# Kernel tuning notes

Hardware: AMD Instinct MI355X
Metric: run time of the kernel (lower is better)

## Reference

```python
import jax, jax.numpy as jnp
import numpy as np

E = 1024   # embd_size
H = 16     # head_count
HS = E // H
B = 8
T = 1024   # seq len == input_size
EPS = 1e-5

def _ln(x, g, b):
    m = jnp.mean(x, axis=-1, keepdims=True)
    v = jnp.mean((x - m) ** 2, axis=-1, keepdims=True)
    return (x - m) * jax.lax.rsqrt(v + EPS) * g + b

def setup_inputs() -> dict:
    key = jax.random.key(0)
    ks = jax.random.split(key, 12)
    s_attn = 1.0 / np.sqrt(E)
    s_ff1 = 1.0 / np.sqrt(E)
    s_ff2 = 1.0 / np.sqrt(4 * E)
    return {
        "x": jax.random.normal(ks[0], (B, T, E), dtype=jnp.float32),
        "wq": jax.random.normal(ks[1], (H, E, HS), dtype=jnp.float32) * s_attn,
        "wk": jax.random.normal(ks[2], (H, E, HS), dtype=jnp.float32) * s_attn,
        "wv": jax.random.normal(ks[3], (H, E, HS), dtype=jnp.float32) * s_attn,
        "w_proj": jax.random.normal(ks[4], (E, E), dtype=jnp.float32) * s_attn,
        "b_proj": jnp.zeros((E,), dtype=jnp.float32),
        "w1": jax.random.normal(ks[5], (E, 4 * E), dtype=jnp.float32) * s_ff1,
        "b1": jnp.zeros((4 * E,), dtype=jnp.float32),
        "w2": jax.random.normal(ks[6], (4 * E, E), dtype=jnp.float32) * s_ff2,
        "b2": jnp.zeros((E,), dtype=jnp.float32),
        "g1": jnp.ones((E,), dtype=jnp.float32),
        "be1": jnp.zeros((E,), dtype=jnp.float32),
        "g2": jnp.ones((E,), dtype=jnp.float32),
        "be2": jnp.zeros((E,), dtype=jnp.float32),
    }

def reference(x, wq, wk, wv, w_proj, b_proj, w1, b1, w2, b2, g1, be1, g2, be2):
    Tn = x.shape[1]
    h = _ln(x, g1, be1)
    # per-head projections, batched over heads: [B,T,E] x [H,E,S] -> [B,H,T,S]
    q = jnp.einsum('bte,hes->bhts', h, wq)
    k = jnp.einsum('bte,hes->bhts', h, wk)
    v = jnp.einsum('bte,hes->bhts', h, wv)
    scores = jnp.einsum('bhts,bhus->bhtu', q, k)
    # NOTE: source multiplies by sqrt(T) (x.shape[2] of scores), not 1/sqrt(head_size)
    scores = scores * jnp.float32(Tn) ** 0.5
    causal = jnp.tril(jnp.ones((Tn, Tn), dtype=bool))
    scores = jnp.where(causal, scores, -jnp.inf)
    attn = jax.nn.softmax(scores, axis=-1)
    out = jnp.einsum('bhtu,bhus->bhts', attn, v)           # [B,H,T,S]
    out = out.transpose(0, 2, 1, 3).reshape(x.shape[0], Tn, E)  # concat heads
    out = out @ w_proj + b_proj
    x = x + out
    f = _ln(x, g2, be2)
    f = jax.nn.relu(f @ w1 + b1) @ w2 + b2
    return x + f
```

## Files before the change

kernel.cpp:

```cpp
#include <hip/hip_runtime.h>


typedef unsigned short u16;
typedef __attribute__((ext_vector_type(8))) short  bfx8;
typedef __attribute__((ext_vector_type(4))) float  f32x4;
typedef __attribute__((ext_vector_type(4))) unsigned short u16v4;

#define MFMA16 __builtin_amdgcn_mfma_f32_16x16x32_bf16

__device__ __forceinline__ u16 f2bf(float f) {
    union { float f; unsigned u; } c; c.f = f;
    unsigned r = c.u + 0x7fffu + ((c.u >> 16) & 1u);
    return (u16)(r >> 16);
}
__device__ __forceinline__ float bf2f(u16 b) {
    union { unsigned u; float f; } c; c.u = ((unsigned)b) << 16; return c.f;
}
__device__ __forceinline__ float exp2_fast(float x) {
    float r; asm("v_exp_f32 %0, %1" : "=v"(r) : "v"(x)); return r;
}

__device__ __forceinline__ void gl_lds16(const void* g, void* l) {
    void* gg = (void*)g;
    __builtin_amdgcn_global_load_lds(
        (__attribute__((address_space(1))) void*)gg,
        (__attribute__((address_space(3))) void*)l,
        16, 0, 0);
}

__global__ __launch_bounds__(256)
void transpose_split(const float* __restrict__ src, u16* __restrict__ dhi,
                     u16* __restrict__ dlo, int C, int OS,
                     size_t inBS, size_t outBS)
{
    __shared__ float t[64][65];
    const int tid = threadIdx.x;
    const float* s = src + (size_t)blockIdx.z * inBS
                   + ((size_t)blockIdx.y * 64) * C + (size_t)blockIdx.x * 64;
    const size_t obase = (size_t)blockIdx.z * outBS
                       + ((size_t)blockIdx.x * 64) * OS + (size_t)blockIdx.y * 64;
    {
        const int r = tid >> 2, c4 = (tid & 3) * 16;
#pragma unroll
        for (int k = 0; k < 4; ++k) {
            float4 f = *(const float4*)(s + (size_t)r * C + c4 + k * 4);
            t[r][c4 + k*4 + 0] = f.x; t[r][c4 + k*4 + 1] = f.y;
            t[r][c4 + k*4 + 2] = f.z; t[r][c4 + k*4 + 3] = f.w;
        }
    }
    __syncthreads();
    {
        const int c = tid >> 2, r4 = (tid & 3) * 16;
        bfx8 h0, h1, l0, l1;
#pragma unroll
        for (int k = 0; k < 8; ++k) {
            float v0 = t[r4 + k][c];
            float v1 = t[r4 + 8 + k][c];
            u16 a = f2bf(v0), b = f2bf(v1);
            h0[k] = (short)a; h1[k] = (short)b;
            l0[k] = (short)f2bf(v0 - bf2f(a));
            l1[k] = (short)f2bf(v1 - bf2f(b));
        }
        u16* d = dhi + obase + (size_t)c * OS + r4;
        *(bfx8*)d = h0; *(bfx8*)(d + 8) = h1;
        if (dlo) {
            u16* d2 = dlo + obase + (size_t)c * OS + r4;
            *(bfx8*)d2 = l0; *(bfx8*)(d2 + 8) = l1;
        }
    }
}

__global__ __launch_bounds__(256)
void transpose_v(const u16* __restrict__ v, u16* __restrict__ vT)
{
    const int ut = blockIdx.x, h = blockIdx.y, b = blockIdx.z;
    __shared__ u16 t[64][72];
    const int tid = threadIdx.x;
    {
        const int u = tid >> 2, s4 = (tid & 3) * 16;
        const u16* src = v + ((size_t)(b * 1024 + ut * 64 + u)) * 1024 + h * 64 + s4;
        bfx8 a = *(const bfx8*)src;
        bfx8 c = *(const bfx8*)(src + 8);
#pragma unroll
        for (int k = 0; k < 8; ++k) { t[u][s4 + k] = (u16)a[k]; t[u][s4 + 8 + k] = (u16)c[k]; }
    }
    __syncthreads();
    {
        const int s = tid >> 2, u4 = (tid & 3) * 16;
        bfx8 o0, o1;
#pragma unroll
        for (int k = 0; k < 8; ++k) { o0[k] = (short)t[u4 + k][s]; o1[k] = (short)t[u4 + 8 + k][s]; }
        u16* dst = vT + ((size_t)((b * 16 + h) * 64 + s)) * 1024 + ut * 64 + u4;
        *(bfx8*)dst = o0; *(bfx8*)(dst + 8) = o1;
    }
}

__global__ __launch_bounds__(256)
void ln_split(const float* __restrict__ x, const float* __restrict__ g,
              const float* __restrict__ be, u16* __restrict__ hhi,
              u16* __restrict__ hlo)
{
    const int row = blockIdx.x;
    const int tid = threadIdx.x;
    const float4 v = ((const float4*)(x + (size_t)row * 1024))[tid];
    float s  = v.x + v.y + v.z + v.w;
    float s2 = v.x*v.x + v.y*v.y + v.z*v.z + v.w*v.w;
#pragma unroll
    for (int m = 32; m >= 1; m >>= 1) {
        s  += __shfl_xor(s,  m, 64);
        s2 += __shfl_xor(s2, m, 64);
    }
    __shared__ float rs[4], rq[4];
    if ((tid & 63) == 0) { rs[tid >> 6] = s; rq[tid >> 6] = s2; }
    __syncthreads();
    s  = rs[0] + rs[1] + rs[2] + rs[3];
    s2 = rq[0] + rq[1] + rq[2] + rq[3];
    const float mean = s * (1.0f / 1024.0f);
    const float var  = s2 * (1.0f / 1024.0f) - mean * mean;
    const float inv  = rsqrtf(var + 1e-5f);
    const int col0 = tid * 4;
    float hv[4];
    hv[0] = (v.x - mean) * inv * g[col0+0] + be[col0+0];
    hv[1] = (v.y - mean) * inv * g[col0+1] + be[col0+1];
    hv[2] = (v.z - mean) * inv * g[col0+2] + be[col0+2];
    hv[3] = (v.w - mean) * inv * g[col0+3] + be[col0+3];
    u16v4 hb, lb;
#pragma unroll
    for (int k = 0; k < 4; ++k) {
        u16 a = f2bf(hv[k]);
        hb[k] = a;
        lb[k] = f2bf(hv[k] - bf2f(a));
    }
    *(u16v4*)(hhi + (size_t)row * 1024 + col0) = hb;
    if (hlo) *(u16v4*)(hlo + (size_t)row * 1024 + col0) = lb;
}

#define BM 128
#define BN 128
#define BKT 32

template<int FLAGS>
__global__ __launch_bounds__(256, 2)
void gemm_bt(const u16* __restrict__ A, const u16* __restrict__ Bt,
             void* __restrict__ Cout, const float* __restrict__ bias,
             const float* __restrict__ res, int M, int N, int K)
{
    __shared__ u16 As[BM * BKT];
    __shared__ u16 Bs[BN * BKT];
    const int tid  = threadIdx.x;
    const int lane = tid & 63, wave = tid >> 6;
    const int wr = wave >> 1, wc = wave & 1;
    const int li = lane & 15, lg = lane >> 4;
    const size_t m0 = (size_t)blockIdx.y * BM;
    const size_t n0 = (size_t)blockIdx.x * BN;
    f32x4 acc[4][4] = {};

    const int slot0 = tid, slot1 = tid + 256;
    const int r0 = slot0 >> 2, kc0 = (slot0 & 3) * 8;
    const int r1 = slot1 >> 2, kc1 = (slot1 & 3) * 8;

    for (int kt = 0; kt < K; kt += BKT) {
        __syncthreads();
        gl_lds16(A  + (m0 + r0) * K + kt + kc0, As + slot0 * 8);
        gl_lds16(Bt + (n0 + r0) * K + kt + kc0, Bs + slot0 * 8);
        gl_lds16(A  + (m0 + r1) * K + kt + kc1, As + slot1 * 8);
        gl_lds16(Bt + (n0 + r1) * K + kt + kc1, Bs + slot1 * 8);
        __syncthreads();
        bfx8 af[4], bfr[4];
#pragma unroll
        for (int i = 0; i < 4; ++i)
            af[i] = *(const bfx8*)&As[(wr * 64 + i * 16 + li) * BKT + lg * 8];
#pragma unroll
        for (int j = 0; j < 4; ++j)
            bfr[j] = *(const bfx8*)&Bs[(wc * 64 + j * 16 + li) * BKT + lg * 8];
#pragma unroll
        for (int i = 0; i < 4; ++i)
#pragma unroll
            for (int j = 0; j < 4; ++j)
                acc[i][j] = MFMA16(af[i], bfr[j], acc[i][j], 0, 0, 0);
    }

    float* Cf = (float*)Cout;
    u16*   Cb = (u16*)Cout;
#pragma unroll
    for (int i = 0; i < 4; ++i)
#pragma unroll
        for (int j = 0; j < 4; ++j)
#pragma unroll
            for (int r = 0; r < 4; ++r) {
                const size_t row = m0 + wr * 64 + i * 16 + lg * 4 + r;
                const size_t col = n0 + wc * 64 + j * 16 + li;
                float v = acc[i][j][r];
                if (FLAGS & 1) v += bias[col];
                if (FLAGS & 2) v = fmaxf(v, 0.0f);
                if (FLAGS & 4) v += res[row * (size_t)N + col];
                if (FLAGS & 8) Cf[row * (size_t)N + col] = v;
                else           Cb[row * (size_t)N + col] = f2bf(v);
            }
}

__global__ __launch_bounds__(512, 2)
void gemm8_ffn1(const u16* __restrict__ A, const u16* __restrict__ Bt,
                u16* __restrict__ C, const float* __restrict__ bias,
                int M, int N, int K)
{
    __shared__ u16 Asl[2][2][128 * 64];
    __shared__ u16 Bsl[2][2][128 * 64];
    const int tid = threadIdx.x;
    const int lane = tid & 63, wave = tid >> 6;
    const int wr = wave >> 2, wc = wave & 3;
    const int li = lane & 15, lg = lane >> 4;

    const int bid = blockIdx.x;
    const int swz = (bid & 7) * 64 + (bid >> 3);
    const int bx = swz & 15, by = swz >> 4;
    const size_t m0 = (size_t)by * 256, n0 = (size_t)bx * 256;

    char* ldsA = (char*)&Asl[0][0][0];
    char* ldsB = (char*)&Bsl[0][0][0];

    auto stageA = [&](int j, int h) {
#pragma unroll
        for (int site = 0; site < 2; ++site) {
            const int s = tid + site * 512;
            const int r = s >> 3;
            const int cb = ((s & 7) << 4) ^ ((r & 7) << 4);
            gl_lds16((const char*)(A + (m0 + h * 128 + r) * (size_t)K + (size_t)j * 64) + cb,
                     ldsA + ((j & 1) * 2 + h) * 16384 + s * 16);
        }
    };
    auto stageB = [&](int j, int h) {
#pragma unroll
        for (int site = 0; site < 2; ++site) {
            const int s = tid + site * 512;
            const int r = s >> 3;
            const int cb = ((s & 7) << 4) ^ ((r & 7) << 4);
            gl_lds16((const char*)(Bt + (n0 + h * 128 + r) * (size_t)K + (size_t)j * 64) + cb,
                     ldsB + ((j & 1) * 2 + h) * 16384 + s * 16);
        }
    };

    const int lsw = (li & 7) << 4;
    const int aHalfBase = wr * 16384;
    const int bHalfBase = (wc >> 1) * 16384;
    const int bRow0 = (wc & 1) * 64;

    f32x4 acc[8][4] = {};
    const int NT = K >> 6;
    const int NI = NT >> 1;

    stageA(0, 0); stageA(0, 1); stageB(0, 0); stageB(0, 1);
    stageB(1, 0); stageB(1, 1);
    asm volatile("s_waitcnt vmcnt(0)" ::: "memory");
    __builtin_amdgcn_sched_barrier(0);
    __builtin_amdgcn_s_barrier();
    __builtin_amdgcn_sched_barrier(0);

    for (int t = 0; t < NI; ++t) {
        const bool more = (t + 1 < NI);
#pragma unroll
        for (int half = 0; half < 2; ++half) {
            const int buf = half;
            const int abase = buf * 32768 + aHalfBase;
            const int bbase = buf * 32768 + bHalfBase;
            bfx8 bfr[4][2];
#pragma unroll
            for (int q = 0; q < 4; ++q) {
                if (q == 0) {
#pragma unroll
                    for (int nf = 0; nf < 4; ++nf)
#pragma unroll
                        for (int ks = 0; ks < 2; ++ks)
                            bfr[nf][ks] = *(const bfx8*)(ldsB + bbase
                                + (bRow0 + nf * 16 + li) * 128
                                + ((ks * 64 + lg * 16) ^ lsw));
                }
                bfx8 afr[2][2];
#pragma unroll
                for (int m = 0; m < 2; ++m)
#pragma unroll
                    for (int ks = 0; ks < 2; ++ks)
                        afr[m][ks] = *(const bfx8*)(ldsA + abase
                            + ((2 * q + m) * 16 + li) * 128
                            + ((ks * 64 + lg * 16) ^ lsw));

                if (half == 0) {
                    if (q == 0) stageA(2 * t + 1, 0);
                    else if (q == 1) stageA(2 * t + 1, 1);
                    else if (q == 2) { if (more) stageB(2 * t + 2, 0); }
                    else             { if (more) stageB(2 * t + 2, 1); }
                } else {
                    if (q == 0)      { if (more) stageA(2 * t + 2, 0); }
                    else if (q == 1) { if (more) stageA(2 * t + 2, 1); }
                    else if (q == 2) { if (more) stageB(2 * t + 3, 0); }
                    else             { if (more) stageB(2 * t + 3, 1); }
                }

                __builtin_amdgcn_sched_barrier(0);
                __builtin_amdgcn_s_barrier();
                asm volatile("s_waitcnt lgkmcnt(0)" ::: "memory");
                __builtin_amdgcn_sched_barrier(0);
                __builtin_amdgcn_s_setprio(1);
#pragma unroll
                for (int ks = 0; ks < 2; ++ks)
#pragma unroll
                    for (int m = 0; m < 2; ++m)
#pragma unroll
                        for (int nf = 0; nf < 4; ++nf)
                            acc[2 * q + m][nf] = MFMA16(afr[m][ks], bfr[nf][ks],
                                                        acc[2 * q + m][nf], 0, 0, 0);
                __builtin_amdgcn_s_setprio(0);
                __builtin_amdgcn_sched_barrier(0);
                if (q == 3) {
                    if (half == 0) {
                        if (more) { asm volatile("s_waitcnt vmcnt(4)" ::: "memory"); }
                        else      { asm volatile("s_waitcnt vmcnt(0)" ::: "memory"); }
                    } else if (more) {
                        asm volatile("s_waitcnt vmcnt(4)" ::: "memory");
                    }
                    __builtin_amdgcn_sched_barrier(0);
                }
                __builtin_amdgcn_s_barrier();
                __builtin_amdgcn_sched_barrier(0);
            }
        }
    }

#pragma unroll
    for (int i = 0; i < 8; ++i)
#pragma unroll
        for (int nf = 0; nf < 4; ++nf)
#pragma unroll
            for (int r = 0; r < 4; ++r) {
                const size_t row = m0 + wr * 128 + i * 16 + lg * 4 + r;
                const size_t col = n0 + wc * 64 + nf * 16 + li;
                float v = acc[i][nf][r] + bias[col];
                v = fmaxf(v, 0.0f);
                C[row * (size_t)N + col] = f2bf(v);
            }
}

__global__ __launch_bounds__(256, 2)
void gemm_qk(const u16* __restrict__ Ah, const u16* __restrict__ Al,
             const u16* __restrict__ Bh, const u16* __restrict__ Bl,
             u16* __restrict__ Ohi, u16* __restrict__ Olo,
             int M, int N, int K)
{
    __shared__ u16 Ahs[BM * BKT], Als[BM * BKT], Bhs[BN * BKT], Bls[BN * BKT];
    const int tid  = threadIdx.x;
    const int lane = tid & 63, wave = tid >> 6;
    const int wr = wave >> 1, wc = wave & 1;
    const int li = lane & 15, lg = lane >> 4;
    const size_t m0 = (size_t)blockIdx.y * BM;
    const size_t n0 = (size_t)blockIdx.x * BN;
    f32x4 acc[4][4] = {};

    const int slot0 = tid, slot1 = tid + 256;
    const int r0 = slot0 >> 2, kc0 = (slot0 & 3) * 8;
    const int r1 = slot1 >> 2, kc1 = (slot1 & 3) * 8;

    for (int kt = 0; kt < K; kt += BKT) {
        __syncthreads();
        gl_lds16(Ah + (m0 + r0) * K + kt + kc0, Ahs + slot0 * 8);
        gl_lds16(Al + (m0 + r0) * K + kt + kc0, Als + slot0 * 8);
        gl_lds16(Bh + (n0 + r0) * K + kt + kc0, Bhs + slot0 * 8);
        gl_lds16(Bl + (n0 + r0) * K + kt + kc0, Bls + slot0 * 8);
        gl_lds16(Ah + (m0 + r1) * K + kt + kc1, Ahs + slot1 * 8);
        gl_lds16(Al + (m0 + r1) * K + kt + kc1, Als + slot1 * 8);
        gl_lds16(Bh + (n0 + r1) * K + kt + kc1, Bhs + slot1 * 8);
        gl_lds16(Bl + (n0 + r1) * K + kt + kc1, Bls + slot1 * 8);
        __syncthreads();
        bfx8 ah[4], al4[4], bh[4], bl4[4];
#pragma unroll
        for (int i = 0; i < 4; ++i) {
            ah[i]  = *(const bfx8*)&Ahs[(wr * 64 + i * 16 + li) * BKT + lg * 8];
            al4[i] = *(const bfx8*)&Als[(wr * 64 + i * 16 + li) * BKT + lg * 8];
        }
#pragma unroll
        for (int j = 0; j < 4; ++j) {
            bh[j]  = *(const bfx8*)&Bhs[(wc * 64 + j * 16 + li) * BKT + lg * 8];
            bl4[j] = *(const bfx8*)&Bls[(wc * 64 + j * 16 + li) * BKT + lg * 8];
        }
#pragma unroll
        for (int i = 0; i < 4; ++i)
#pragma unroll
            for (int j = 0; j < 4; ++j) {
                acc[i][j] = MFMA16(ah[i],  bh[j],  acc[i][j], 0, 0, 0);
                acc[i][j] = MFMA16(ah[i],  bl4[j], acc[i][j], 0, 0, 0);
                acc[i][j] = MFMA16(al4[i], bh[j],  acc[i][j], 0, 0, 0);
            }
    }
#pragma unroll
    for (int i = 0; i < 4; ++i)
#pragma unroll
        for (int j = 0; j < 4; ++j)
#pragma unroll
            for (int r = 0; r < 4; ++r) {
                const size_t row = m0 + wr * 64 + i * 16 + lg * 4 + r;
                const size_t col = n0 + wc * 64 + j * 16 + li;
                const float v = acc[i][j][r];
                const u16 hi = f2bf(v);
                Ohi[row * (size_t)N + col] = hi;
                Olo[row * (size_t)N + col] = f2bf(v - bf2f(hi));
            }
}

__global__ __launch_bounds__(256, 3)
void attn(const u16* __restrict__ qhi, const u16* __restrict__ qlo,
          const u16* __restrict__ khi, const u16* __restrict__ klo,
          const u16* __restrict__ vt, u16* __restrict__ ao)
{
    const int id  = blockIdx.x;
    const int swz = (id & 7) * 256 + (id >> 3);
    const int qt  = 15 - (swz & 15);
    const int h   = (swz >> 4) & 15;
    const int b   = swz >> 8;

    const int tid = threadIdx.x;
    const int wave = tid >> 6, lane = tid & 63;
    const int li = lane & 15, lg = lane >> 4;

    __shared__ u16 KsHi[2][4096];
    __shared__ u16 KsLo[2][4096];
    __shared__ u16 Pl[64 * 72];

    const size_t qrow = (size_t)b * 1024 + qt * 64 + wave * 16 + li;
    const size_t qoff = qrow * 1024 + h * 64 + lg * 8;
    const bfx8 qh0 = *(const bfx8*)(qhi + qoff);
    const bfx8 qh1 = *(const bfx8*)(qhi + qoff + 32);
    const bfx8 ql0 = *(const bfx8*)(qlo + qoff);
    const bfx8 ql1 = *(const bfx8*)(qlo + qoff + 32);

    f32x4 O[4] = {};
    float mrow[4] = {-1e30f, -1e30f, -1e30f, -1e30f};
    float lrow[4] = {0.f, 0.f, 0.f, 0.f};

    const int vs  = tid >> 2;
    const int vu4 = (tid & 3) * 16;
    (void)vs; (void)vu4;

    const u16* kh_base = khi + ((size_t)b * 1024) * 1024 + h * 64;
    const u16* kl_base = klo + ((size_t)b * 1024) * 1024 + h * 64;
    const u16* v_base  = vt + ((size_t)(b * 16 + h) * 64) * 1024;

    auto stageK = [&](int kt, int bufIdx) {
#pragma unroll
        for (int site = 0; site < 2; ++site) {
            const int s = tid + site * 256;
            const int r = s >> 3;
            const int cb = (((s & 7) << 4) ^ ((r & 7) << 4));
            const size_t go = ((size_t)(kt * 64 + r)) * 1024;
            gl_lds16((const char*)(kh_base + go) + cb, (char*)&KsHi[bufIdx][0] + s * 16);
            gl_lds16((const char*)(kl_base + go) + cb, (char*)&KsLo[bufIdx][0] + s * 16);
        }
    };

    const int rswz = (li & 7) << 4;

    stageK(0, 0);

    for (int kt = 0; kt <= qt; ++kt) {
        const int cur = kt & 1;

        bfx8 vld[2][4];
#pragma unroll
        for (int nf = 0; nf < 4; ++nf) {
            const u16* vr = v_base + ((size_t)(nf * 16 + li)) * 1024 + kt * 64 + lg * 8;
            vld[0][nf] = *(const bfx8*)vr;
            vld[1][nf] = *(const bfx8*)(vr + 32);
        }

        if (kt < qt) {
            stageK(kt + 1, cur ^ 1);
            asm volatile("s_waitcnt vmcnt(12)" ::: "memory");
        } else {
            asm volatile("s_waitcnt vmcnt(8)" ::: "memory");
        }
        __builtin_amdgcn_sched_barrier(0);
        __builtin_amdgcn_s_barrier();
        __builtin_amdgcn_sched_barrier(0);

        float sv[4][4];
        const char* khc = (const char*)&KsHi[cur][0];
        const char* klc = (const char*)&KsLo[cur][0];
#pragma unroll
        for (int nf = 0; nf < 4; ++nf) {
            const int rb = (nf * 16 + li) * 128;
            bfx8 kh0v = *(const bfx8*)(khc + rb + (((lg * 16) + 0 ) ^ rswz));
            bfx8 kh1v = *(const bfx8*)(khc + rb + (((lg * 16) + 64) ^ rswz));
            bfx8 kl0v = *(const bfx8*)(klc + rb + (((lg * 16) + 0 ) ^ rswz));
            bfx8 kl1v = *(const bfx8*)(klc + rb + (((lg * 16) + 64) ^ rswz));
            f32x4 a = {0.f, 0.f, 0.f, 0.f};
            a = MFMA16(qh0, kh0v, a, 0, 0, 0);
            a = MFMA16(qh1, kh1v, a, 0, 0, 0);
            a = MFMA16(qh0, kl0v, a, 0, 0, 0);
            a = MFMA16(qh1, kl1v, a, 0, 0, 0);
            a = MFMA16(ql0, kh0v, a, 0, 0, 0);
            a = MFMA16(ql1, kh1v, a, 0, 0, 0);
#pragma unroll
            for (int r = 0; r < 4; ++r) sv[nf][r] = a[r];
        }

        asm volatile("s_waitcnt lgkmcnt(0)" ::: "memory");
        __builtin_amdgcn_sched_barrier(0);
        __builtin_amdgcn_s_barrier();
        __builtin_amdgcn_sched_barrier(0);

        const int rowg = qt * 64 + wave * 16 + lg * 4;
        const int colg = kt * 64 + li;
        float pmax[4] = {-1e30f, -1e30f, -1e30f, -1e30f};
#pragma unroll
        for (int nf = 0; nf < 4; ++nf)
#pragma unroll
            for (int r = 0; r < 4; ++r) {
                float x2 = sv[nf][r] * 46.166240905715613f;
                if (colg + nf * 16 > rowg + r) x2 = -1e30f;
                sv[nf][r] = x2;
                pmax[r] = fmaxf(pmax[r], x2);
            }
#pragma unroll
        for (int msk = 1; msk < 16; msk <<= 1)
#pragma unroll
            for (int r = 0; r < 4; ++r)
                pmax[r] = fmaxf(pmax[r], __shfl_xor(pmax[r], msk, 64));

        float alr[4], rsum[4];
#pragma unroll
        for (int r = 0; r < 4; ++r) {
            const float mnew = fmaxf(mrow[r], pmax[r]);
            alr[r] = exp2_fast(mrow[r] - mnew);
            mrow[r] = mnew;
            rsum[r] = 0.0f;
        }
        float pv[4][4];
#pragma unroll
        for (int nf = 0; nf < 4; ++nf)
#pragma unroll
            for (int r = 0; r < 4; ++r) {
                const float p = exp2_fast(sv[nf][r] - mrow[r]);
                pv[nf][r] = p;
                rsum[r] += p;
            }
#pragma unroll
        for (int msk = 1; msk < 16; msk <<= 1)
#pragma unroll
            for (int r = 0; r < 4; ++r)
                rsum[r] += __shfl_xor(rsum[r], msk, 64);
#pragma unroll
        for (int r = 0; r < 4; ++r)
            lrow[r] = lrow[r] * alr[r] + rsum[r];
#pragma unroll
        for (int nf = 0; nf < 4; ++nf)
#pragma unroll
            for (int r = 0; r < 4; ++r)
                O[nf][r] *= alr[r];

#pragma unroll
        for (int nf = 0; nf < 4; ++nf)
#pragma unroll
            for (int r = 0; r < 4; ++r)
                Pl[(wave * 16 + lg * 4 + r) * 72 + nf * 16 + li] = f2bf(pv[nf][r]);

#pragma unroll
        for (int ku = 0; ku < 2; ++ku) {
            bfx8 pf = *(const bfx8*)&Pl[(wave * 16 + li) * 72 + ku * 32 + lg * 8];
#pragma unroll
            for (int nf = 0; nf < 4; ++nf)
                O[nf] = MFMA16(pf, vld[ku][nf], O[nf], 0, 0, 0);
        }
    }

    float invl[4];
#pragma unroll
    for (int r = 0; r < 4; ++r) invl[r] = 1.0f / lrow[r];
    const size_t orow = (size_t)b * 1024 + qt * 64 + wave * 16 + lg * 4;
#pragma unroll
    for (int nf = 0; nf < 4; ++nf)
#pragma unroll
        for (int r = 0; r < 4; ++r)
            ao[(orow + r) * 1024 + h * 64 + nf * 16 + li] = f2bf(O[nf][r] * invl[r]);
}

extern "C" void kernel_launch(void* const* d_in, const int* in_sizes, int n_in,
                              void* d_out, int out_size, void* d_ws, size_t ws_size,
                              hipStream_t stream)
{
    (void)in_sizes; (void)n_in; (void)out_size; (void)ws_size;
    const float* x      = (const float*)d_in[0];
    const float* wq     = (const float*)d_in[1];
    const float* wk     = (const float*)d_in[2];
    const float* wv     = (const float*)d_in[3];
    const float* w_proj = (const float*)d_in[4];
    const float* b_proj = (const float*)d_in[5];
    const float* w1     = (const float*)d_in[6];
    const float* b1     = (const float*)d_in[7];
    const float* w2     = (const float*)d_in[8];
    const float* b2     = (const float*)d_in[9];
    const float* g1     = (const float*)d_in[10];
    const float* be1    = (const float*)d_in[11];
    const float* g2     = (const float*)d_in[12];
    const float* be2    = (const float*)d_in[13];
    float* out = (float*)d_out;

    const size_t ME2 = (size_t)8192 * 1024 * 2;
    char* wsp = (char*)d_ws;
    u16* h_hi = (u16*)(wsp + 0 * ME2);
    u16* h_lo = (u16*)(wsp + 1 * ME2);
    u16* q_hi = (u16*)(wsp + 2 * ME2);
    u16* q_lo = (u16*)(wsp + 3 * ME2);
    u16* k_hi = (u16*)(wsp + 4 * ME2);
    u16* k_lo = (u16*)(wsp + 5 * ME2);
    u16* v_b  = (u16*)(wsp + 6 * ME2);
    u16* vtr  = (u16*)(wsp + 7 * ME2);
    float* y  = (float*)(wsp + 8 * ME2);
    char* wp0 = wsp + 8 * ME2 + (size_t)8192 * 1024 * 4;
    const size_t W1M = (size_t)1024 * 1024 * 2;
    u16* wqT_hi = (u16*)(wp0 + 0 * W1M);
    u16* wqT_lo = (u16*)(wp0 + 1 * W1M);
    u16* wkT_hi = (u16*)(wp0 + 2 * W1M);
    u16* wkT_lo = (u16*)(wp0 + 3 * W1M);
    u16* wvT    = (u16*)(wp0 + 4 * W1M);
    u16* wpT    = (u16*)(wp0 + 5 * W1M);
    u16* w1T    = (u16*)(wp0 + 6 * W1M);
    u16* w2T    = (u16*)(wp0 + 6 * W1M + 4 * W1M);
    u16* f2  = h_hi;
    u16* ao  = h_lo;
    u16* act = q_hi;

    dim3 blk(256);

    transpose_split<<<dim3(1, 16, 16), blk, 0, stream>>>(wq, wqT_hi, wqT_lo, 64, 1024, (size_t)65536, (size_t)65536);
    transpose_split<<<dim3(1, 16, 16), blk, 0, stream>>>(wk, wkT_hi, wkT_lo, 64, 1024, (size_t)65536, (size_t)65536);
    transpose_split<<<dim3(1, 16, 16), blk, 0, stream>>>(wv, wvT, nullptr, 64, 1024, (size_t)65536, (size_t)65536);
    transpose_split<<<dim3(16, 16, 1), blk, 0, stream>>>(w_proj, wpT, nullptr, 1024, 1024, 0, 0);
    transpose_split<<<dim3(64, 16, 1), blk, 0, stream>>>(w1, w1T, nullptr, 4096, 1024, 0, 0);
    transpose_split<<<dim3(16, 64, 1), blk, 0, stream>>>(w2, w2T, nullptr, 1024, 4096, 0, 0);

    ln_split<<<8192, blk, 0, stream>>>(x, g1, be1, h_hi, h_lo);

    gemm_qk<<<dim3(8, 64), blk, 0, stream>>>(h_hi, h_lo, wqT_hi, wqT_lo, q_hi, q_lo, 8192, 1024, 1024);
    gemm_qk<<<dim3(8, 64), blk, 0, stream>>>(h_hi, h_lo, wkT_hi, wkT_lo, k_hi, k_lo, 8192, 1024, 1024);
    gemm_bt<0><<<dim3(8, 64), blk, 0, stream>>>(h_hi, wvT, v_b, nullptr, nullptr, 8192, 1024, 1024);
    transpose_v<<<dim3(16, 16, 8), blk, 0, stream>>>(v_b, vtr);

    attn<<<dim3(2048), blk, 0, stream>>>(q_hi, q_lo, k_hi, k_lo, vtr, ao);

    gemm_bt<1 | 4 | 8><<<dim3(8, 64), blk, 0, stream>>>(ao, wpT, y, b_proj, x, 8192, 1024, 1024);

    ln_split<<<8192, blk, 0, stream>>>(y, g2, be2, f2, nullptr);

    gemm8_ffn1<<<dim3(512), dim3(512), 0, stream>>>(f2, w1T, act, b1, 8192, 4096, 1024);
    gemm_bt<1 | 4 | 8><<<dim3(8, 64), blk, 0, stream>>>(act, w2T, out, b2, y, 8192, 1024, 4096);
}
```

Baseline: 546.8 us.

## Lazy softmax rescaling, MFMA row-sum, and mask only diagonal tiles in attention

In the flash-attention loop, the causal mask is now applied only on the diagonal tile. The running max is updated, and O rescaled, only when some row's new max exceeds the old one by more than a threshold (wave-uniform vote). The row-sum shuffle reduction is replaced by an extra MFMA against a ones vector, which accumulates the denominator from the same bf16 P values. This removes per-tile exp/shuffle work, at the cost of unnormalized exponents that can grow up to 2^11.5 and an extra MFMA per k-step.

```diff
diff --git a/kernel.cpp b/kernel.cpp
--- a/kernel.cpp
+++ b/kernel.cpp
@@ -431,13 +431,13 @@
     const bfx8 ql0 = *(const bfx8*)(qlo + qoff);
     const bfx8 ql1 = *(const bfx8*)(qlo + qoff + 32);
 
+    bfx8 onesf;
+#pragma unroll
+    for (int k = 0; k < 8; ++k) onesf[k] = (short)0x3F80;
+
     f32x4 O[4] = {};
-    float mrow[4] = {-1e30f, -1e30f, -1e30f, -1e30f};
-    float lrow[4] = {0.f, 0.f, 0.f, 0.f};
-
-    const int vs  = tid >> 2;
-    const int vu4 = (tid & 3) * 16;
-    (void)vs; (void)vu4;
+    f32x4 O5 = {0.f, 0.f, 0.f, 0.f};
+    float mrow[4] = {-3e38f, -3e38f, -3e38f, -3e38f};
 
     const u16* kh_base = khi + ((size_t)b * 1024) * 1024 + h * 64;
     const u16* kl_base = klo + ((size_t)b * 1024) * 1024 + h * 64;
@@ -506,60 +506,64 @@
         __builtin_amdgcn_s_barrier();
         __builtin_amdgcn_sched_barrier(0);
 
-        const int rowg = qt * 64 + wave * 16 + lg * 4;
-        const int colg = kt * 64 + li;
-        float pmax[4] = {-1e30f, -1e30f, -1e30f, -1e30f};
-#pragma unroll
-        for (int nf = 0; nf < 4; ++nf)
-#pragma unroll
-            for (int r = 0; r < 4; ++r) {
-                float x2 = sv[nf][r] * 46.166240905715613f;
-                if (colg + nf * 16 > rowg + r) x2 = -1e30f;
-                sv[nf][r] = x2;
-                pmax[r] = fmaxf(pmax[r], x2);
-            }
+        const float SC = 46.16624130844683f;
+        float pmax[4] = {-3e38f, -3e38f, -3e38f, -3e38f};
+        if (kt == qt) {
+            const int rowg = qt * 64 + wave * 16 + lg * 4;
+            const int colg = kt * 64 + li;
+#pragma unroll
+            for (int nf = 0; nf < 4; ++nf)
+#pragma unroll
+                for (int r = 0; r < 4; ++r) {
+                    float x2 = sv[nf][r] * SC;
+                    if (colg + nf * 16 > rowg + r) x2 = -3e38f;
+                    sv[nf][r] = x2;
+                    pmax[r] = fmaxf(pmax[r], x2);
+                }
+        } else {
+#pragma unroll
+            for (int nf = 0; nf < 4; ++nf)
+#pragma unroll
+                for (int r = 0; r < 4; ++r) {
+                    const float x2 = sv[nf][r] * SC;
+                    sv[nf][r] = x2;
+                    pmax[r] = fmaxf(pmax[r], x2);
+                }
+        }
 #pragma unroll
         for (int msk = 1; msk < 16; msk <<= 1)
 #pragma unroll
             for (int r = 0; r < 4; ++r)
                 pmax[r] = fmaxf(pmax[r], __shfl_xor(pmax[r], msk, 64));
 
-        float alr[4], rsum[4];
-#pragma unroll
-        for (int r = 0; r < 4; ++r) {
-            const float mnew = fmaxf(mrow[r], pmax[r]);
-            alr[r] = exp2_fast(mrow[r] - mnew);
-            mrow[r] = mnew;
-            rsum[r] = 0.0f;
-        }
-        float pv[4][4];
+        const bool grow = !__all((pmax[0] - mrow[0] <= 11.5416f) &&
+                                 (pmax[1] - mrow[1] <= 11.5416f) &&
+                                 (pmax[2] - mrow[2] <= 11.5416f) &&
+                                 (pmax[3] - mrow[3] <= 11.5416f));
+        if (grow) {
+            float alr[4];
+#pragma unroll
+            for (int r = 0; r < 4; ++r) {
+                const float mnew = fmaxf(mrow[r], pmax[r]);
+                alr[r] = exp2_fast(mrow[r] - mnew);
+                mrow[r] = mnew;
+            }
+#pragma unroll
+            for (int nf = 0; nf < 4; ++nf)
+#pragma unroll
+                for (int r = 0; r < 4; ++r)
+                    O[nf][r] *= alr[r];
+#pragma unroll
+            for (int r = 0; r < 4; ++r)
+                O5[r] *= alr[r];
+        }
+
 #pragma unroll
         for (int nf = 0; nf < 4; ++nf)
 #pragma unroll
-            for (int r = 0; r < 4; ++r) {
-                const float p = exp2_fast(sv[nf][r] - mrow[r]);
-                pv[nf][r] = p;
-                rsum[r] += p;
-            }
-#pragma unroll
-        for (int msk = 1; msk < 16; msk <<= 1)
-#pragma unroll
             for (int r = 0; r < 4; ++r)
-                rsum[r] += __shfl_xor(rsum[r], msk, 64);
-#pragma unroll
-        for (int r = 0; r < 4; ++r)
-            lrow[r] = lrow[r] * alr[r] + rsum[r];
-#pragma unroll
-        for (int nf = 0; nf < 4; ++nf)
-#pragma unroll
-            for (int r = 0; r < 4; ++r)
-                O[nf][r] *= alr[r];
-
-#pragma unroll
-        for (int nf = 0; nf < 4; ++nf)
-#pragma unroll
-            for (int r = 0; r < 4; ++r)
-                Pl[(wave * 16 + lg * 4 + r) * 72 + nf * 16 + li] = f2bf(pv[nf][r]);
+                Pl[(wave * 16 + lg * 4 + r) * 72 + nf * 16 + li] =
+                    f2bf(exp2_fast(sv[nf][r] - mrow[r]));
 
 #pragma unroll
         for (int ku = 0; ku < 2; ++ku) {
@@ -567,12 +571,13 @@
 #pragma unroll
             for (int nf = 0; nf < 4; ++nf)
                 O[nf] = MFMA16(pf, vld[ku][nf], O[nf], 0, 0, 0);
+            O5 = MFMA16(pf, onesf, O5, 0, 0, 0);
         }
     }
 
     float invl[4];
 #pragma unroll
-    for (int r = 0; r < 4; ++r) invl[r] = 1.0f / lrow[r];
+    for (int r = 0; r < 4; ++r) invl[r] = 1.0f / O5[r];
     const size_t orow = (size_t)b * 1024 + qt * 64 + wave * 16 + lg * 4;
 #pragma unroll
     for (int nf = 0; nf < 4; ++nf)
```

New measurement: 539.0 us. Within noise of the previous version (-1.4%).
